# Performance work log

Hardware: AMD Instinct MI355X
Metric: run time of the kernel (lower is better)

The kernel has to match this reference:

```python
import jax, jax.numpy as jnp
import numpy as np
from jax import lax

B, T, D, U = 64, 2048, 512, 32


def setup_inputs() -> dict:
    key = jax.random.key(0)
    k1, k2, k3, k4 = jax.random.split(key, 4)
    x = jax.random.normal(k1, (B, T, D), dtype=jnp.float32)
    # sequence lengths in [1, T]
    nwords = jnp.maximum(jax.random.randint(k2, (B,), 0, T, dtype=jnp.int32), 1)
    kernel = jax.random.normal(k3, (D, U), dtype=jnp.float32) * 0.02
    chain_kernel = jax.random.normal(k4, (U, U), dtype=jnp.float32) * 0.02
    bias = jnp.zeros((U,), dtype=jnp.float32)
    return {"x": x, "nwords": nwords, "kernel": kernel,
            "chain_kernel": chain_kernel, "bias": bias}


def _crf_decode(logits, trans, lengths):
    """Viterbi decode. logits [B,T,U], trans [U,U], lengths [B] int.
    Returns (pred_ids [B,T] int32, best_score [B])."""
    Bb, Tt, Uu = logits.shape
    alpha0 = logits[:, 0]                       # [B,U]
    # valid[t-1, b] = (t < lengths[b]) for t = 1..T-1
    valid = (jnp.arange(1, Tt)[:, None] < lengths[None, :])  # [T-1, B]
    logits_rest = jnp.transpose(logits[:, 1:], (1, 0, 2))    # [T-1, B, U]
    tag_iota = jnp.arange(Uu, dtype=jnp.int32)

    def fwd_step(alpha, inp):
        logit_t, v = inp                        # [B,U], [B]
        scores = alpha[:, :, None] + trans[None, :, :]   # [B, U_prev, U_cur]
        bp = jnp.argmax(scores, axis=1).astype(jnp.int32)  # [B,U]
        new_alpha = jnp.max(scores, axis=1) + logit_t        # [B,U]
        new_alpha = jnp.where(v[:, None], new_alpha, alpha)
        bp = jnp.where(v[:, None], bp, tag_iota[None, :])    # identity at pads
        return new_alpha, bp

    final_alpha, bps = lax.scan(fwd_step, alpha0, (logits_rest, valid))
    # bps: [T-1, B, U]
    last_tag = jnp.argmax(final_alpha, axis=-1).astype(jnp.int32)  # [B]
    best_score = jnp.max(final_alpha, axis=-1)                     # [B]

    def back_step(tag, bp_t):
        prev_tag = jnp.take_along_axis(bp_t, tag[:, None], axis=1)[:, 0]
        return prev_tag, tag

    first_tag, tags_rest = lax.scan(back_step, last_tag, bps, reverse=True)
    # tags_rest[t-1] = tag at time t; first_tag = tag at time 0
    pred = jnp.concatenate([first_tag[None, :], tags_rest], axis=0)  # [T,B]
    return jnp.transpose(pred, (1, 0)), best_score


def reference(x, nwords, kernel, chain_kernel, bias):
    # dense projection (activation = linear, keras default)
    logits = jnp.einsum('btd,du->btu', x, kernel) + bias  # [B,T,U]
    pred_ids, best_score = _crf_decode(logits, chain_kernel, nwords)
    return pred_ids, best_score
```

## Files before the change

### kernel.cpp

```cpp
#include <hip/hip_runtime.h>

#define BB 64
#define TT 2048
#define DD 512
#define UU 32

__device__ int g_ts[BB * 3];
__device__ float g_c[BB * 3];

__global__ __launch_bounds__(256, 4) void k1_logits(const float* __restrict__ x,
                                                    const float* __restrict__ w,
                                                    const float* __restrict__ bias,
                                                    float* __restrict__ out) {
  __shared__ float xs[128 * 34];
  __shared__ float wsh[32 * 36];
  const int tid = threadIdx.x;
  const long row0 = (long)blockIdx.x * 128;
  const int tr = tid >> 2;
  const int tc = tid & 3;
  const int ubase = tc * 8;
  const int sr = tid >> 3;
  const int sc = (tid & 7) * 4;

  float2 acc2[2][4];
#pragma unroll
  for (int i = 0; i < 2; ++i)
#pragma unroll
    for (int j = 0; j < 4; ++j) acc2[i][j] = make_float2(0.0f, 0.0f);

  for (int kc = 0; kc < DD; kc += 32) {
#pragma unroll
    for (int p = 0; p < 4; ++p) {
      const int r = p * 32 + sr;
      const float4 v = *(const float4*)(x + (row0 + r) * DD + kc + sc);
      *(float2*)(&xs[r * 34 + sc]) = make_float2(v.x, v.y);
      *(float2*)(&xs[r * 34 + sc + 2]) = make_float2(v.z, v.w);
    }
    {
      const int k = tid >> 3;
      const int uu4 = (tid & 7) * 4;
      const float4 v = *(const float4*)(w + (size_t)(kc + k) * UU + uu4);
      *(float4*)(&wsh[k * 36 + uu4]) = v;
    }
    __syncthreads();
#pragma unroll
    for (int kp = 0; kp < 16; ++kp) {
      const int k = kp * 2;
      const float4 wa0 = *(const float4*)(&wsh[k * 36 + ubase]);
      const float4 wa1 = *(const float4*)(&wsh[k * 36 + ubase + 4]);
      const float4 wb0 = *(const float4*)(&wsh[(k + 1) * 36 + ubase]);
      const float4 wb1 = *(const float4*)(&wsh[(k + 1) * 36 + ubase + 4]);
#pragma unroll
      for (int i = 0; i < 2; ++i) {
        const float2 xv2 = *(const float2*)(&xs[(tr + 64 * i) * 34 + k]);
        acc2[i][0].x = fmaf(xv2.x, wa0.x, acc2[i][0].x);
        acc2[i][0].y = fmaf(xv2.x, wa0.y, acc2[i][0].y);
        acc2[i][1].x = fmaf(xv2.x, wa0.z, acc2[i][1].x);
        acc2[i][1].y = fmaf(xv2.x, wa0.w, acc2[i][1].y);
        acc2[i][2].x = fmaf(xv2.x, wa1.x, acc2[i][2].x);
        acc2[i][2].y = fmaf(xv2.x, wa1.y, acc2[i][2].y);
        acc2[i][3].x = fmaf(xv2.x, wa1.z, acc2[i][3].x);
        acc2[i][3].y = fmaf(xv2.x, wa1.w, acc2[i][3].y);
        acc2[i][0].x = fmaf(xv2.y, wb0.x, acc2[i][0].x);
        acc2[i][0].y = fmaf(xv2.y, wb0.y, acc2[i][0].y);
        acc2[i][1].x = fmaf(xv2.y, wb0.z, acc2[i][1].x);
        acc2[i][1].y = fmaf(xv2.y, wb0.w, acc2[i][1].y);
        acc2[i][2].x = fmaf(xv2.y, wb1.x, acc2[i][2].x);
        acc2[i][2].y = fmaf(xv2.y, wb1.y, acc2[i][2].y);
        acc2[i][3].x = fmaf(xv2.y, wb1.z, acc2[i][3].x);
        acc2[i][3].y = fmaf(xv2.y, wb1.w, acc2[i][3].y);
      }
    }
    __syncthreads();
  }
  float bv[8];
#pragma unroll
  for (int j = 0; j < 8; ++j) bv[j] = bias[ubase + j];
#pragma unroll
  for (int i = 0; i < 2; ++i) {
    const long row = row0 + tr + 64 * i;
    float4 o0, o1;
    o0.x = acc2[i][0].x + bv[0]; o0.y = acc2[i][0].y + bv[1];
    o0.z = acc2[i][1].x + bv[2]; o0.w = acc2[i][1].y + bv[3];
    o1.x = acc2[i][2].x + bv[4]; o1.y = acc2[i][2].y + bv[5];
    o1.z = acc2[i][3].x + bv[6]; o1.w = acc2[i][3].y + bv[7];
    *(float4*)(out + row * UU + ubase) = o0;
    *(float4*)(out + row * UU + ubase + 4) = o1;
  }
}


#define ROTF(S) \
  __int_as_float(__builtin_amdgcn_update_dpp(0, __float_as_int(P), 0x120 + (S), 0xF, 0xF, true))

#define K2_TREE                                                              \
    const float c0 = P + tvS[0];                                             \
    const float c1 = ROTF(1) + tvS[1];                                       \
    const float c2 = ROTF(2) + tvS[2];                                       \
    const float c3 = ROTF(3) + tvS[3];                                       \
    const float c4 = ROTF(4) + tvS[4];                                       \
    const float c5 = ROTF(5) + tvS[5];                                       \
    const float c6 = ROTF(6) + tvS[6];                                       \
    const float c7 = ROTF(7) + tvS[7];                                       \
    const float c8 = ROTF(8) + tvS[8];                                       \
    const float c9 = ROTF(9) + tvS[9];                                       \
    const float c10 = ROTF(10) + tvS[10];                                    \
    const float c11 = ROTF(11) + tvS[11];                                    \
    const float c12 = ROTF(12) + tvS[12];                                    \
    const float c13 = ROTF(13) + tvS[13];                                    \
    const float c14 = ROTF(14) + tvS[14];                                    \
    const float c15 = ROTF(15) + tvS[15];                                    \
    const float d0 = fmaxf(fmaxf(c0, c1), c2);                               \
    const float d1 = fmaxf(fmaxf(c3, c4), c5);                               \
    const float d2 = fmaxf(fmaxf(c6, c7), c8);                               \
    const float d3 = fmaxf(fmaxf(c9, c10), c11);                             \
    const float d4 = fmaxf(fmaxf(c12, c13), c14);                            \
    const float e0 = fmaxf(fmaxf(d0, d1), d2);                               \
    const float e1 = fmaxf(fmaxf(d3, d4), c15);                              \
    const float pm = fmaxf(e0, e1);

#if __has_builtin(__builtin_amdgcn_permlane32_swap) && __has_builtin(__builtin_amdgcn_permlane16_swap)
#define K2_HAVE_PERMLANE 1
typedef unsigned int v2u __attribute__((ext_vector_type(2)));

#define K2_FSTEP(tval, lg) do {                                              \
    K2_TREE                                                                  \
    v2u s32 = __builtin_amdgcn_permlane32_swap(__float_as_uint(pm),          \
                                               __float_as_uint(pm), false, false); \
    const float pd = fmaxf(__uint_as_float(s32.x), __uint_as_float(s32.y)) + (lg); \
    v2u s16 = __builtin_amdgcn_permlane16_swap(__float_as_uint(pd),          \
                                               __float_as_uint(pd), false, false); \
    const float cx = m16sel ? __uint_as_float(s16.x) : __uint_as_float(s16.y); \
    P = bit5v ? cx : pd;                                                     \
    base[(size_t)(tval) * UU + cstoS] = P;                                   \
  } while (0)

__device__ __forceinline__ float k2_mcomb(float P, const float* tvS) {
  K2_TREE
  v2u s32 = __builtin_amdgcn_permlane32_swap(__float_as_uint(pm),
                                             __float_as_uint(pm), false, false);
  return fmaxf(__uint_as_float(s32.x), __uint_as_float(s32.y));
}
#endif

__global__ __launch_bounds__(64) void k2a_forward(float* __restrict__ lb,
                                                  const float* __restrict__ trans) {
  const int lane = threadIdx.x;
  const int q = lane & 15;
  const int bit4 = (lane >> 4) & 1;
  const int bit5v = (lane >> 5) & 1;
  const int hiS = bit4 ^ bit5v;
  const int tgtS = bit4 * 16 + q;
  const int cstoS = hiS * 16 + q;
  const int role = blockIdx.x >> 6;
  const int b = blockIdx.x & 63;

  const int probe = __builtin_amdgcn_update_dpp(0, q, 0x121, 0xF, 0xF, false);
  const bool dirp = (probe == ((q + 1) & 15));

  float tvS[16];
#pragma unroll
  for (int s = 0; s < 16; ++s) {
    const int rp = dirp ? ((q + s) & 15) : ((q - s) & 15);
    tvS[s] = trans[(hiS * 16 + rp) * UU + tgtS];
  }

  float* base = lb + (size_t)b * TT * UU;
  float bufA[16], bufB[16];

#ifdef K2_HAVE_PERMLANE
  v2u p32 = __builtin_amdgcn_permlane32_swap((unsigned)lane, (unsigned)lane, false, false);
  v2u p16 = __builtin_amdgcn_permlane16_swap((unsigned)lane, (unsigned)lane, false, false);
  const bool c32ok = ((int)p32.x == (lane ^ 32)) || ((int)p32.y == (lane ^ 32));
  const bool c16ok = ((int)p16.x == (lane ^ 16)) || ((int)p16.y == (lane ^ 16));
  const bool m16sel = ((int)p16.x == (lane ^ 16));
  const bool okSwap = (__ballot(c32ok) == ~0ull) && (__ballot(c16ok) == ~0ull);

  if (okSwap) {
    if (role == 0) {
      float P = base[cstoS];
#pragma unroll
      for (int i = 0; i < 16; ++i) bufA[i] = base[(size_t)(1 + i) * UU + tgtS];
#pragma unroll 1
      for (int tc = 1; tc <= 481; tc += 32) {
#pragma unroll
        for (int i = 0; i < 16; ++i) bufB[i] = base[(size_t)(tc + 16 + i) * UU + tgtS];
#pragma unroll
        for (int i = 0; i < 16; ++i) K2_FSTEP(tc + i, bufA[i]);
#pragma unroll
        for (int i = 0; i < 16; ++i) bufA[i] = base[(size_t)(tc + 32 + i) * UU + tgtS];
#pragma unroll
        for (int i = 0; i < 16; ++i) K2_FSTEP(tc + 16 + i, bufB[i]);
      }
    } else {
      const int s0 = 512 * role + 1;
      const int A = s0 + 1;
      const int E = (role < 3) ? (512 * (role + 1)) : (TT - 1);
      float P = base[(size_t)s0 * UU + cstoS];
#pragma unroll
      for (int i = 0; i < 16; ++i) bufA[i] = base[(size_t)(A + i) * UU + tgtS];
#pragma unroll 1
      for (int tc = A; tc <= A + 448; tc += 32) {
#pragma unroll
        for (int i = 0; i < 16; ++i) bufB[i] = base[(size_t)(tc + 16 + i) * UU + tgtS];
#pragma unroll
        for (int i = 0; i < 16; ++i) K2_FSTEP(tc + i, bufA[i]);
#pragma unroll
        for (int i = 0; i < 16; ++i) bufA[i] = base[(size_t)(tc + 32 + i) * UU + tgtS];
#pragma unroll
        for (int i = 0; i < 16; ++i) K2_FSTEP(tc + 16 + i, bufB[i]);
      }
      const int tailN = E - (A + 496) + 1;
#pragma unroll
      for (int i = 0; i < 16; ++i) {
        int r = A + 496 + i; if (r > E) r = E;
        bufB[i] = base[(size_t)r * UU + tgtS];
      }
#pragma unroll
      for (int i = 0; i < 16; ++i) K2_FSTEP(A + 480 + i, bufA[i]);
      for (int i = 0; i < tailN; ++i) K2_FSTEP(A + 496 + i, bufB[i]);
    }
    return;
  }
#endif

  if (role != 0) return;
  {
    float tvD[16];
#pragma unroll
    for (int s = 0; s < 16; ++s) {
      const int rp = dirp ? ((q + s) & 15) : ((q - s) & 15);
      tvD[s] = trans[(bit4 * 16 + rp) * UU + cstoS];
    }
    const int idx32 = (lane ^ 32) << 2;
    const int idx48 = (lane ^ 48) << 2;
    float P = base[cstoS];

#define K2_BSTEP(tval, lg, TVHI, XIDX, SCOL) do {                            \
    const float g0 = P + (TVHI)[0];                                          \
    const float g1 = ROTF(1) + (TVHI)[1];                                    \
    const float g2 = ROTF(2) + (TVHI)[2];                                    \
    const float g3 = ROTF(3) + (TVHI)[3];                                    \
    const float g4 = ROTF(4) + (TVHI)[4];                                    \
    const float g5 = ROTF(5) + (TVHI)[5];                                    \
    const float g6 = ROTF(6) + (TVHI)[6];                                    \
    const float g7 = ROTF(7) + (TVHI)[7];                                    \
    const float g8 = ROTF(8) + (TVHI)[8];                                    \
    const float g9 = ROTF(9) + (TVHI)[9];                                    \
    const float g10 = ROTF(10) + (TVHI)[10];                                 \
    const float g11 = ROTF(11) + (TVHI)[11];                                 \
    const float g12 = ROTF(12) + (TVHI)[12];                                 \
    const float g13 = ROTF(13) + (TVHI)[13];                                 \
    const float g14 = ROTF(14) + (TVHI)[14];                                 \
    const float g15 = ROTF(15) + (TVHI)[15];                                 \
    const float h0 = fmaxf(fmaxf(g0, g1), g2);                               \
    const float h1 = fmaxf(fmaxf(g3, g4), g5);                               \
    const float h2 = fmaxf(fmaxf(g6, g7), g8);                               \
    const float h3 = fmaxf(fmaxf(g9, g10), g11);                             \
    const float h4 = fmaxf(fmaxf(g12, g13), g14);                            \
    const float k0 = fmaxf(fmaxf(h0, h1), h2);                               \
    const float k1 = fmaxf(fmaxf(h3, h4), g15);                              \
    const float pm2 = fmaxf(k0, k1);                                         \
    const int po = __builtin_amdgcn_ds_bpermute((XIDX), __float_as_int(pm2));\
    P = fmaxf(pm2, __int_as_float(po)) + (lg);                               \
    base[(size_t)(tval) * UU + (SCOL)] = P;                                  \
  } while (0)

#pragma unroll
    for (int i = 0; i < 16; ++i)
      bufA[i] = base[(size_t)(1 + i) * UU + ((i & 1) ? cstoS : tgtS)];
#pragma unroll 1
    for (int tc = 1; tc <= 1985; tc += 32) {
#pragma unroll
      for (int i = 0; i < 16; ++i)
        bufB[i] = base[(size_t)(tc + 16 + i) * UU + ((i & 1) ? cstoS : tgtS)];
#pragma unroll
      for (int i = 0; i < 16; ++i) {
        if ((i & 1) == 0) K2_BSTEP(tc + i, bufA[i], tvS, idx32, tgtS);
        else              K2_BSTEP(tc + i, bufA[i], tvD, idx48, cstoS);
      }
#pragma unroll
      for (int i = 0; i < 16; ++i)
        bufA[i] = base[(size_t)(tc + 32 + i) * UU + ((i & 1) ? cstoS : tgtS)];
#pragma unroll
      for (int i = 0; i < 16; ++i) {
        if ((i & 1) == 0) K2_BSTEP(tc + 16 + i, bufB[i], tvS, idx32, tgtS);
        else              K2_BSTEP(tc + 16 + i, bufB[i], tvD, idx48, cstoS);
      }
    }
#pragma unroll
    for (int i = 0; i < 16; ++i) {
      int r = 2033 + i; if (r > TT - 1) r = TT - 1;
      bufB[i] = base[(size_t)r * UU + ((i & 1) ? cstoS : tgtS)];
    }
#pragma unroll
    for (int i = 0; i < 16; ++i) {
      if ((i & 1) == 0) K2_BSTEP(2017 + i, bufA[i], tvS, idx32, tgtS);
      else              K2_BSTEP(2017 + i, bufA[i], tvD, idx48, cstoS);
    }
#pragma unroll
    for (int i = 0; i < 15; ++i) {
      if ((i & 1) == 0) K2_BSTEP(2033 + i, bufB[i], tvS, idx32, tgtS);
      else              K2_BSTEP(2033 + i, bufB[i], tvD, idx48, cstoS);
    }
  }
}

__global__ __launch_bounds__(64) void k2b_fixup(float* __restrict__ lb,
                                                const float* __restrict__ trans) {
  const int lane = threadIdx.x;
  const int b = blockIdx.x;
  const int q = lane & 15;
  const int bit4 = (lane >> 4) & 1;
  const int bit5v = (lane >> 5) & 1;
  const int hiS = bit4 ^ bit5v;
  const int tgtS = bit4 * 16 + q;
  const int cstoS = hiS * 16 + q;

  const int probe = __builtin_amdgcn_update_dpp(0, q, 0x121, 0xF, 0xF, false);
  const bool dirp = (probe == ((q + 1) & 15));

  float tvS[16];
#pragma unroll
  for (int s = 0; s < 16; ++s) {
    const int rp = dirp ? ((q + s) & 15) : ((q - s) & 15);
    tvS[s] = trans[(hiS * 16 + rp) * UU + tgtS];
  }

#ifdef K2_HAVE_PERMLANE
  v2u p32 = __builtin_amdgcn_permlane32_swap((unsigned)lane, (unsigned)lane, false, false);
  v2u p16 = __builtin_amdgcn_permlane16_swap((unsigned)lane, (unsigned)lane, false, false);
  const bool c32ok = ((int)p32.x == (lane ^ 32)) || ((int)p32.y == (lane ^ 32));
  const bool c16ok = ((int)p16.x == (lane ^ 16)) || ((int)p16.y == (lane ^ 16));
  const bool m16sel = ((int)p16.x == (lane ^ 16));
  const bool okSwap = (__ballot(c32ok) == ~0ull) && (__ballot(c16ok) == ~0ull);
  if (!okSwap) {
    if (lane == 0) {
#pragma unroll
      for (int j = 0; j < 3; ++j) { g_ts[b * 3 + j] = (j < 2) ? (1024 + 512 * j) : (TT - 1); g_c[b * 3 + j] = 0.0f; }
    }
    return;
  }

  float* base = lb + (size_t)b * TT * UU;
  const float TAU = 0.05f;
  float trueP = base[(size_t)512 * UU + cstoS];

#pragma unroll 1
  for (int j = 0; j < 3; ++j) {
    const int jr = 513 + 512 * j;
    const int segEnd = (j < 2) ? (1024 + 512 * j) : (TT - 1);
    const float specInit = base[(size_t)jr * UU + cstoS];
    const float lgj = base[(size_t)jr * UU + tgtS];
    { float P = trueP; K2_FSTEP(jr, lgj); trueP = P; }
    float specP = specInit;

    float ring[4];
#pragma unroll
    for (int i = 0; i < 4; ++i) {
      int r = jr + 1 + i; if (r > segEnd) r = segEnd;
      ring[i] = base[(size_t)r * UU + cstoS];
    }
    int ts_rec = segEnd; float c_rec = 0.0f;
#pragma unroll 1
    for (int t = jr + 1; t <= segEnd; ++t) {
      const float specRow = ring[(t - (jr + 1)) & 3];
      const int pf = t + 4;
      if (pf <= segEnd) ring[(t - (jr + 1)) & 3] = base[(size_t)pf * UU + cstoS];
      const float Mt = k2_mcomb(trueP, tvS);
      const float Ms = k2_mcomb(specP, tvS);
      const float d = Mt - Ms;
      v2u s16d = __builtin_amdgcn_permlane16_swap(__float_as_uint(d),
                                                  __float_as_uint(d), false, false);
      const float dx = m16sel ? __uint_as_float(s16d.x) : __uint_as_float(s16d.y);
      const float dsel = bit5v ? dx : d;
      const float nt = specRow + dsel;
      base[(size_t)t * UU + cstoS] = nt;
      const float dref = __uint_as_float(
          (unsigned)__builtin_amdgcn_readfirstlane(__float_as_int(d)));
      const bool uni = (__ballot(fabsf(d - dref) <= TAU) == ~0ull);
      trueP = nt;
      specP = specRow;
      if (uni) { ts_rec = t; c_rec = dref; break; }
    }
    if (lane == 0) { g_ts[b * 3 + j] = ts_rec; g_c[b * 3 + j] = c_rec; }
    if (ts_rec < segEnd) {
      trueP = base[(size_t)segEnd * UU + cstoS] + c_rec;
    }
  }
#else
  if (lane == 0) {
#pragma unroll
    for (int j = 0; j < 3; ++j) { g_ts[b * 3 + j] = (j < 2) ? (1024 + 512 * j) : (TT - 1); g_c[b * 3 + j] = 0.0f; }
  }
#endif
}

__global__ __launch_bounds__(256) void k2c_apply(float* __restrict__ lb) {
  const int b = blockIdx.x;
#pragma unroll 1
  for (int j = 0; j < 3; ++j) {
    const int ts = g_ts[b * 3 + j];
    const int segEnd = (j < 2) ? (1024 + 512 * j) : (TT - 1);
    const float c = g_c[b * 3 + j];
    if (c == 0.0f || ts >= segEnd) continue;
    const int r0 = ts + 1;
    float4* p = (float4*)(lb + ((size_t)b * TT + r0) * UU);
    const int n4 = (segEnd - r0 + 1) * (UU / 4);
    for (int i = threadIdx.x; i < n4; i += 256) {
      float4 v = p[i];
      v.x += c; v.y += c; v.z += c; v.w += c;
      p[i] = v;
    }
  }
}

__global__ __launch_bounds__(256) void k3_bp(const float* __restrict__ lb,
                                             const float* __restrict__ trans,
                                             const int* __restrict__ nwords,
                                             unsigned char* __restrict__ bp) {
  __shared__ float as[129 * 32];
  __shared__ float ts[32 * 32];
  const int b = blockIdx.x >> 4;
  const int c = blockIdx.x & 15;
  const int t0 = 128 * c;
  const int tid = threadIdx.x;
  const float* base = lb + (size_t)b * TT * UU;
  const int nw = nwords[b];

  for (int idx = tid; idx < 129 * 32; idx += 256) {
    const int gidx = (t0 - 1) * 32 + idx;
    as[idx] = (gidx >= 0 && gidx < TT * UU) ? base[gidx] : 0.0f;
  }
  for (int idx = tid; idx < 1024; idx += 256) ts[idx] = trans[idx];
  __syncthreads();

  const int u = tid & 31;
  const int tg = tid >> 5;
  unsigned char* bpu = bp + ((size_t)b * 32 + u) * TT;

#pragma unroll 1
  for (int qq = 0; qq < 4; ++qq) {
    const int tl0 = tg * 16 + qq * 4;
    unsigned int pack = 0;
#pragma unroll
    for (int e = 0; e < 4; ++e) {
      const int tl = tl0 + e;
      const int t = t0 + tl;
      int idx;
      if (t >= 1 && t < nw) {
        float m = as[tl * 32 + 0] + ts[0 * 32 + u];
        idx = 0;
#pragma unroll
        for (int v = 1; v < 32; ++v) {
          const float cv = as[tl * 32 + v] + ts[v * 32 + u];
          if (cv > m) { m = cv; idx = v; }
        }
      } else {
        idx = u;
      }
      pack |= ((unsigned int)idx) << (8 * e);
    }
    *(unsigned int*)(bpu + t0 + tl0) = pack;
  }
}

__global__ __launch_bounds__(64) void k4_backtrace(const float* __restrict__ lb,
                                                   const unsigned char* __restrict__ bp,
                                                   const int* __restrict__ nwords,
                                                   int* __restrict__ pred,
                                                   float* __restrict__ score) {
  const int b = blockIdx.x;
  const int lane = threadIdx.x;
  const int u = lane & 31;
  const int h = lane >> 5;
  const int nw = nwords[b];

  const float a = lb[((size_t)b * TT + (nw - 1)) * UU + u];
  float m = a;
#pragma unroll
  for (int s = 32; s; s >>= 1) m = fmaxf(m, __shfl_xor(m, s));
  if (lane == 0) score[b] = m;
  const unsigned long long mask = __ballot(lane < 32 && a == m);
  int tag = __ffsll((unsigned long long)mask) - 1;
  tag = __builtin_amdgcn_readfirstlane(tag);

  int* predb = pred + b * TT;
  for (int p = nw - 1 + lane; p < TT; p += 64) predb[p] = tag;
  if (nw < 2) return;

  const unsigned char* bpb = bp + (size_t)b * 32 * TT;
  const int pcmax = (nw - 2) >> 6;
  const int thi_top = nw - 1;

  int wprev0 = 0;
  {
    const int toff = (pcmax + 1) * 64;
    if (toff < TT) wprev0 = *(const int*)(bpb + (size_t)u * TT + toff);
  }

  for (int pc = pcmax; pc >= 0; --pc) {
    int wreg[8];
#pragma unroll
    for (int j = 0; j < 8; ++j)
      wreg[j] = *(const int*)(bpb + (size_t)u * TT + pc * 64 + 4 * (h * 8 + j));
    int predv = 0;

    if (pc == pcmax) {
      const int thi = thi_top;
      if (pc * 64 + 64 <= thi) {
        const int val = __builtin_amdgcn_readlane(wprev0, tag);
        tag = __builtin_amdgcn_readfirstlane(val & 0xFF);
        if (lane == 63) predv = tag;
      }
#pragma unroll
      for (int lt = 63; lt >= 1; --lt) {
        if (pc * 64 + lt <= thi) {
          const int d = lt >> 2, byte = lt & 3;
          const int hs = d >> 3, j = d & 7;
          const int val = __builtin_amdgcn_readlane(wreg[j], hs * 32 + tag);
          tag = __builtin_amdgcn_readfirstlane((val >> (8 * byte)) & 0xFF);
          if (lane == lt - 1) predv = tag;
        }
      }
      const int lim = thi - pc * 64;
      if (lane < lim) predb[pc * 64 + lane] = predv;
    } else {
      {
        const int val = __builtin_amdgcn_readlane(wprev0, tag);
        tag = __builtin_amdgcn_readfirstlane(val & 0xFF);
        if (lane == 63) predv = tag;
      }
#pragma unroll
      for (int lt = 63; lt >= 1; --lt) {
        const int d = lt >> 2, byte = lt & 3;
        const int hs = d >> 3, j = d & 7;
        const int val = __builtin_amdgcn_readlane(wreg[j], hs * 32 + tag);
        tag = __builtin_amdgcn_readfirstlane((val >> (8 * byte)) & 0xFF);
        if (lane == lt - 1) predv = tag;
      }
      predb[pc * 64 + lane] = predv;
    }
    wprev0 = wreg[0];
  }
}

extern "C" void kernel_launch(void* const* d_in, const int* in_sizes, int n_in,
                              void* d_out, int out_size, void* d_ws, size_t ws_size,
                              hipStream_t stream) {
  const float* x = (const float*)d_in[0];
  const int* nwords = (const int*)d_in[1];
  const float* kern = (const float*)d_in[2];
  const float* chain = (const float*)d_in[3];
  const float* bias = (const float*)d_in[4];

  float* logits = (float*)d_ws;
  unsigned char* bp = (unsigned char*)d_ws + (size_t)BB * TT * UU * 4;

  int* pred = (int*)d_out;
  float* score = (float*)d_out + (size_t)BB * TT;

  k1_logits<<<dim3(1024), dim3(256), 0, stream>>>(x, kern, bias, logits);
  k2a_forward<<<dim3(256), dim3(64), 0, stream>>>(logits, chain);
  k2b_fixup<<<dim3(BB), dim3(64), 0, stream>>>(logits, chain);
  k2c_apply<<<dim3(BB), dim3(256), 0, stream>>>(logits);
  k3_bp<<<dim3(BB * 16), dim3(256), 0, stream>>>(logits, chain, nwords, bp);
  k4_backtrace<<<dim3(BB), dim3(64), 0, stream>>>(logits, bp, nwords, pred, score);
}
```

Measured before the change: 209.9 us.

## Split Viterbi forward into eight speculative segments with parallel per-segment fixup

The speculative forward pass now splits the sequence into eight 256-step segments instead of four 512-step ones, launching 512 forward blocks. Each segment's end state is saved to a global boundary buffer. The fixup kernel no longer walks the three segments one after another in a single block; it runs one block per segment and batch, starting from the saved speculative boundary. The apply kernel then uses a prefix sum of the per-segment offsets to correct the values. This shortens the serial critical path of the forward recurrence and of the fixup. The cost is more fixup work, and correctness now rests on the assumption that the offset between speculative and true alpha converges within each shorter segment, with errors adding across segment boundaries.

Result: faster. 192.2 us (-8.4%).

```diff
diff --git a/kernel.cpp b/kernel.cpp
--- a/kernel.cpp
+++ b/kernel.cpp
@@ -5,8 +5,9 @@
 #define DD 512
 #define UU 32
 
-__device__ int g_ts[BB * 3];
-__device__ float g_c[BB * 3];
+__device__ int g_ts[BB * 7];
+__device__ float g_c[BB * 7];
+__device__ float g_bound[BB * 8 * 64];
 
 __global__ __launch_bounds__(256, 4) void k1_logits(const float* __restrict__ x,
                                                     const float* __restrict__ w,
@@ -141,6 +142,41 @@
                                              __float_as_uint(pm), false, false);
   return fmaxf(__uint_as_float(s32.x), __uint_as_float(s32.y));
 }
+
+#define K2_RUNSEG(A_, E_) do {                                               \
+    int tcc = (A_);                                                          \
+    _Pragma("unroll")                                                        \
+    for (int i = 0; i < 16; ++i) {                                           \
+      int r = (A_) + i; if (r > (E_)) r = (E_);                              \
+      bufA[i] = base[(size_t)r * UU + tgtS];                                 \
+    }                                                                        \
+    _Pragma("unroll 1")                                                      \
+    for (; tcc + 31 <= (E_); tcc += 32) {                                    \
+      _Pragma("unroll")                                                      \
+      for (int i = 0; i < 16; ++i) bufB[i] = base[(size_t)(tcc + 16 + i) * UU + tgtS]; \
+      _Pragma("unroll")                                                      \
+      for (int i = 0; i < 16; ++i) K2_FSTEP(tcc + i, bufA[i]);               \
+      _Pragma("unroll")                                                      \
+      for (int i = 0; i < 16; ++i) {                                         \
+        int r = tcc + 32 + i; if (r > (E_)) r = (E_);                        \
+        bufA[i] = base[(size_t)r * UU + tgtS];                               \
+      }                                                                      \
+      _Pragma("unroll")                                                      \
+      for (int i = 0; i < 16; ++i) K2_FSTEP(tcc + 16 + i, bufB[i]);          \
+    }                                                                        \
+    const int rem = (E_) - tcc + 1;                                          \
+    if (rem > 0) {                                                           \
+      _Pragma("unroll")                                                      \
+      for (int i = 0; i < 16; ++i) {                                         \
+        int r = tcc + 16 + i; if (r > (E_)) r = (E_);                        \
+        bufB[i] = base[(size_t)r * UU + tgtS];                               \
+      }                                                                      \
+      _Pragma("unroll")                                                      \
+      for (int i = 0; i < 16; ++i) { if (i < rem) K2_FSTEP(tcc + i, bufA[i]); } \
+      _Pragma("unroll")                                                      \
+      for (int i = 0; i < 16; ++i) { if (16 + i < rem) K2_FSTEP(tcc + 16 + i, bufB[i]); } \
+    }                                                                        \
+  } while (0)
 #endif
 
 __global__ __launch_bounds__(64) void k2a_forward(float* __restrict__ lb,
@@ -179,46 +215,14 @@
   if (okSwap) {
     if (role == 0) {
       float P = base[cstoS];
-#pragma unroll
-      for (int i = 0; i < 16; ++i) bufA[i] = base[(size_t)(1 + i) * UU + tgtS];
-#pragma unroll 1
-      for (int tc = 1; tc <= 481; tc += 32) {
-#pragma unroll
-        for (int i = 0; i < 16; ++i) bufB[i] = base[(size_t)(tc + 16 + i) * UU + tgtS];
-#pragma unroll
-        for (int i = 0; i < 16; ++i) K2_FSTEP(tc + i, bufA[i]);
-#pragma unroll
-        for (int i = 0; i < 16; ++i) bufA[i] = base[(size_t)(tc + 32 + i) * UU + tgtS];
-#pragma unroll
-        for (int i = 0; i < 16; ++i) K2_FSTEP(tc + 16 + i, bufB[i]);
-      }
+      K2_RUNSEG(1, 256);
+      g_bound[((b << 3) + 0) * 64 + lane] = P;
     } else {
-      const int s0 = 512 * role + 1;
-      const int A = s0 + 1;
-      const int E = (role < 3) ? (512 * (role + 1)) : (TT - 1);
+      const int s0 = 256 * role + 1;
+      const int E = (role < 7) ? (256 * (role + 1)) : (TT - 1);
       float P = base[(size_t)s0 * UU + cstoS];
-#pragma unroll
-      for (int i = 0; i < 16; ++i) bufA[i] = base[(size_t)(A + i) * UU + tgtS];
-#pragma unroll 1
-      for (int tc = A; tc <= A + 448; tc += 32) {
-#pragma unroll
-        for (int i = 0; i < 16; ++i) bufB[i] = base[(size_t)(tc + 16 + i) * UU + tgtS];
-#pragma unroll
-        for (int i = 0; i < 16; ++i) K2_FSTEP(tc + i, bufA[i]);
-#pragma unroll
-        for (int i = 0; i < 16; ++i) bufA[i] = base[(size_t)(tc + 32 + i) * UU + tgtS];
-#pragma unroll
-        for (int i = 0; i < 16; ++i) K2_FSTEP(tc + 16 + i, bufB[i]);
-      }
-      const int tailN = E - (A + 496) + 1;
-#pragma unroll
-      for (int i = 0; i < 16; ++i) {
-        int r = A + 496 + i; if (r > E) r = E;
-        bufB[i] = base[(size_t)r * UU + tgtS];
-      }
-#pragma unroll
-      for (int i = 0; i < 16; ++i) K2_FSTEP(A + 480 + i, bufA[i]);
-      for (int i = 0; i < tailN; ++i) K2_FSTEP(A + 496 + i, bufB[i]);
+      K2_RUNSEG(s0 + 1, E);
+      g_bound[((b << 3) + role) * 64 + lane] = P;
     }
     return;
   }
@@ -309,13 +313,16 @@
 __global__ __launch_bounds__(64) void k2b_fixup(float* __restrict__ lb,
                                                 const float* __restrict__ trans) {
   const int lane = threadIdx.x;
-  const int b = blockIdx.x;
+  const int b = blockIdx.x & 63;
+  const int j = (blockIdx.x >> 6) + 1;
   const int q = lane & 15;
   const int bit4 = (lane >> 4) & 1;
   const int bit5v = (lane >> 5) & 1;
   const int hiS = bit4 ^ bit5v;
   const int tgtS = bit4 * 16 + q;
   const int cstoS = hiS * 16 + q;
+  const int jr = 256 * j + 1;
+  const int segEnd = (j < 7) ? (256 * (j + 1)) : (TT - 1);
 
   const int probe = __builtin_amdgcn_update_dpp(0, q, 0x121, 0xF, 0xF, false);
   const bool dirp = (probe == ((q + 1) & 15));
@@ -335,82 +342,83 @@
   const bool m16sel = ((int)p16.x == (lane ^ 16));
   const bool okSwap = (__ballot(c32ok) == ~0ull) && (__ballot(c16ok) == ~0ull);
   if (!okSwap) {
-    if (lane == 0) {
-#pragma unroll
-      for (int j = 0; j < 3; ++j) { g_ts[b * 3 + j] = (j < 2) ? (1024 + 512 * j) : (TT - 1); g_c[b * 3 + j] = 0.0f; }
-    }
+    if (lane == 0) { g_ts[b * 7 + j - 1] = segEnd; g_c[b * 7 + j - 1] = 0.0f; }
     return;
   }
 
   float* base = lb + (size_t)b * TT * UU;
   const float TAU = 0.05f;
-  float trueP = base[(size_t)512 * UU + cstoS];
-
+
+  float trueP = g_bound[((b << 3) + (j - 1)) * 64 + lane];
+  const float specInit = base[(size_t)jr * UU + cstoS];
+  const float lgj = base[(size_t)jr * UU + tgtS];
+  { float P = trueP; K2_FSTEP(jr, lgj); trueP = P; }
+  float specP = specInit;
+
+  float ring[4];
+#pragma unroll
+  for (int i = 0; i < 4; ++i) {
+    int r = jr + 1 + i; if (r > segEnd) r = segEnd;
+    ring[i] = base[(size_t)r * UU + cstoS];
+  }
+  int ts_rec = segEnd; float c_rec = 0.0f;
 #pragma unroll 1
-  for (int j = 0; j < 3; ++j) {
-    const int jr = 513 + 512 * j;
-    const int segEnd = (j < 2) ? (1024 + 512 * j) : (TT - 1);
-    const float specInit = base[(size_t)jr * UU + cstoS];
-    const float lgj = base[(size_t)jr * UU + tgtS];
-    { float P = trueP; K2_FSTEP(jr, lgj); trueP = P; }
-    float specP = specInit;
-
-    float ring[4];
-#pragma unroll
-    for (int i = 0; i < 4; ++i) {
-      int r = jr + 1 + i; if (r > segEnd) r = segEnd;
-      ring[i] = base[(size_t)r * UU + cstoS];
-    }
-    int ts_rec = segEnd; float c_rec = 0.0f;
-#pragma unroll 1
-    for (int t = jr + 1; t <= segEnd; ++t) {
-      const float specRow = ring[(t - (jr + 1)) & 3];
-      const int pf = t + 4;
-      if (pf <= segEnd) ring[(t - (jr + 1)) & 3] = base[(size_t)pf * UU + cstoS];
-      const float Mt = k2_mcomb(trueP, tvS);
-      const float Ms = k2_mcomb(specP, tvS);
-      const float d = Mt - Ms;
-      v2u s16d = __builtin_amdgcn_permlane16_swap(__float_as_uint(d),
-                                                  __float_as_uint(d), false, false);
-      const float dx = m16sel ? __uint_as_float(s16d.x) : __uint_as_float(s16d.y);
-      const float dsel = bit5v ? dx : d;
-      const float nt = specRow + dsel;
-      base[(size_t)t * UU + cstoS] = nt;
-      const float dref = __uint_as_float(
-          (unsigned)__builtin_amdgcn_readfirstlane(__float_as_int(d)));
-      const bool uni = (__ballot(fabsf(d - dref) <= TAU) == ~0ull);
-      trueP = nt;
-      specP = specRow;
-      if (uni) { ts_rec = t; c_rec = dref; break; }
-    }
-    if (lane == 0) { g_ts[b * 3 + j] = ts_rec; g_c[b * 3 + j] = c_rec; }
-    if (ts_rec < segEnd) {
-      trueP = base[(size_t)segEnd * UU + cstoS] + c_rec;
-    }
-  }
+  for (int t = jr + 1; t <= segEnd; ++t) {
+    const float specRow = ring[(t - (jr + 1)) & 3];
+    const int pf = t + 4;
+    if (pf <= segEnd) ring[(t - (jr + 1)) & 3] = base[(size_t)pf * UU + cstoS];
+    const float Mt = k2_mcomb(trueP, tvS);
+    const float Ms = k2_mcomb(specP, tvS);
+    const float d = Mt - Ms;
+    v2u s16d = __builtin_amdgcn_permlane16_swap(__float_as_uint(d),
+                                                __float_as_uint(d), false, false);
+    const float dx = m16sel ? __uint_as_float(s16d.x) : __uint_as_float(s16d.y);
+    const float dsel = bit5v ? dx : d;
+    const float nt = specRow + dsel;
+    base[(size_t)t * UU + cstoS] = nt;
+    const float dref = __uint_as_float(
+        (unsigned)__builtin_amdgcn_readfirstlane(__float_as_int(d)));
+    const bool uni = (__ballot(fabsf(d - dref) <= TAU) == ~0ull);
+    trueP = nt;
+    specP = specRow;
+    if (uni) { ts_rec = t; c_rec = dref; break; }
+  }
+  if (lane == 0) { g_ts[b * 7 + j - 1] = ts_rec; g_c[b * 7 + j - 1] = c_rec; }
 #else
-  if (lane == 0) {
-#pragma unroll
-    for (int j = 0; j < 3; ++j) { g_ts[b * 3 + j] = (j < 2) ? (1024 + 512 * j) : (TT - 1); g_c[b * 3 + j] = 0.0f; }
-  }
+  if (lane == 0) { g_ts[b * 7 + j - 1] = segEnd; g_c[b * 7 + j - 1] = 0.0f; }
 #endif
 }
 
 __global__ __launch_bounds__(256) void k2c_apply(float* __restrict__ lb) {
   const int b = blockIdx.x;
+  float C[8];
+  C[0] = 0.0f;
+#pragma unroll
+  for (int j = 1; j <= 7; ++j) C[j] = C[j - 1] + g_c[b * 7 + j - 1];
 #pragma unroll 1
-  for (int j = 0; j < 3; ++j) {
-    const int ts = g_ts[b * 3 + j];
-    const int segEnd = (j < 2) ? (1024 + 512 * j) : (TT - 1);
-    const float c = g_c[b * 3 + j];
-    if (c == 0.0f || ts >= segEnd) continue;
-    const int r0 = ts + 1;
-    float4* p = (float4*)(lb + ((size_t)b * TT + r0) * UU);
-    const int n4 = (segEnd - r0 + 1) * (UU / 4);
-    for (int i = threadIdx.x; i < n4; i += 256) {
-      float4 v = p[i];
-      v.x += c; v.y += c; v.z += c; v.w += c;
-      p[i] = v;
+  for (int j = 1; j <= 7; ++j) {
+    const int jr = 256 * j + 1;
+    const int segEnd = (j < 7) ? (256 * (j + 1)) : (TT - 1);
+    const int ts = g_ts[b * 7 + j - 1];
+    const float cA = C[j - 1];
+    const float cB = C[j];
+    if (cA != 0.0f) {
+      float4* p = (float4*)(lb + ((size_t)b * TT + jr) * UU);
+      const int n4 = (ts - jr + 1) * (UU / 4);
+      for (int i = threadIdx.x; i < n4; i += 256) {
+        float4 v = p[i];
+        v.x += cA; v.y += cA; v.z += cA; v.w += cA;
+        p[i] = v;
+      }
+    }
+    if (cB != 0.0f && ts < segEnd) {
+      float4* p = (float4*)(lb + ((size_t)b * TT + ts + 1) * UU);
+      const int n4 = (segEnd - ts) * (UU / 4);
+      for (int i = threadIdx.x; i < n4; i += 256) {
+        float4 v = p[i];
+        v.x += cB; v.y += cB; v.z += cB; v.w += cB;
+        p[i] = v;
+      }
     }
   }
 }
@@ -561,8 +569,8 @@
   float* score = (float*)d_out + (size_t)BB * TT;
 
   k1_logits<<<dim3(1024), dim3(256), 0, stream>>>(x, kern, bias, logits);
-  k2a_forward<<<dim3(256), dim3(64), 0, stream>>>(logits, chain);
-  k2b_fixup<<<dim3(BB), dim3(64), 0, stream>>>(logits, chain);
+  k2a_forward<<<dim3(512), dim3(64), 0, stream>>>(logits, chain);
+  k2b_fixup<<<dim3(448), dim3(64), 0, stream>>>(logits, chain);
   k2c_apply<<<dim3(BB), dim3(256), 0, stream>>>(logits);
   k3_bp<<<dim3(BB * 16), dim3(256), 0, stream>>>(logits, chain, nwords, bp);
   k4_backtrace<<<dim3(BB), dim3(64), 0, stream>>>(logits, bp, nwords, pred, score);
```
